# Kernel optimization log

Hardware: AMD Instinct MI355X
Metric: run time of the kernel (lower is better)

## Reference

```python
import jax, jax.numpy as jnp
import numpy as np

BATCH = 16384
IN = 1024
OUT = 1024
SIGMA_MIN = 0.1
SIGMA_MAX = 1.0


def setup_inputs() -> dict:
    key = jax.random.key(0)
    k0, k1, k2, k3 = jax.random.split(key, 4)
    x = jax.random.normal(k0, (BATCH, IN), dtype=jnp.float32)
    # torch init: triu(randn) -> upper-triangular reflector banks
    U = jnp.triu(jax.random.normal(k1, (IN, IN), dtype=jnp.float32))
    V = jnp.triu(jax.random.normal(k2, (OUT, OUT), dtype=jnp.float32))
    p = 0.001 * jax.random.normal(k3, (min(IN, OUT),), dtype=jnp.float32)
    bias = jnp.zeros((OUT,), dtype=jnp.float32)
    return {"x": x, "U": U, "V": V, "p": p, "bias": bias}


def _hprod_step(x, u):
    # u has zeros in its first i entries (triu row i), so the full-vector
    # form equals torch's sliced Hprod on the last k = n - i columns.
    alpha = 2.0 * (x @ u) / jnp.dot(u, u)          # [bs]
    return x - alpha[:, None] * u[None, :], None   # rank-1 update


def reference(x, U, V, p, bias):
    r = (SIGMA_MAX - SIGMA_MIN) / 2.0
    sigma_mean = SIGMA_MIN + r
    # mask enforces torch slice semantics (entries below diag never used)
    Um = U * jnp.triu(jnp.ones_like(U))
    Vm = V * jnp.triu(jnp.ones_like(V))
    # Umultiply: reflectors i = 0 .. n_U-1 in order (sequential recurrence)
    x, _ = jax.lax.scan(_hprod_step, x, Um)
    # Sigma: diagonal scaling (square case IN == OUT)
    sigmas = 2.0 * r * (jax.nn.sigmoid(p) - 0.5) + sigma_mean
    x = x * sigmas[None, :]
    # Vmultiply: reflectors i = n_V-1 .. 0 (reverse order)
    x, _ = jax.lax.scan(_hprod_step, x, Vm[::-1])
    return x + bias
```

## Files before the change

### kernel.cpp

```cpp
#include <hip/hip_runtime.h>
#include <stdint.h>

typedef __attribute__((ext_vector_type(8))) short short8;
typedef __attribute__((ext_vector_type(4))) float f32x4;

#define NN 1024
#define NBATCH 16384
#define ME ((size_t)NN * NN)

__device__ __forceinline__ unsigned short f32_to_bf16_rne(float f) {
  unsigned int u = __float_as_uint(f);
  unsigned int r = (u + 0x7fffu + ((u >> 16) & 1u)) >> 16;
  return (unsigned short)r;
}

__device__ __forceinline__ unsigned int pack2bf(float lo, float hi) {
  return (unsigned int)f32_to_bf16_rne(lo) | ((unsigned int)f32_to_bf16_rne(hi) << 16);
}

__device__ __forceinline__ void split_bf16(float x, unsigned short& h, unsigned short& l) {
  h = f32_to_bf16_rne(x);
  float hf = __uint_as_float((unsigned int)h << 16);
  l = f32_to_bf16_rne(x - hf);
}

__device__ __forceinline__ float allsum64(float x) {
  x += __int_as_float(__builtin_amdgcn_update_dpp(0, __float_as_int(x), 0xB1, 0xF, 0xF, true));
  x += __int_as_float(__builtin_amdgcn_update_dpp(0, __float_as_int(x), 0x4E, 0xF, 0xF, true));
  x += __int_as_float(__builtin_amdgcn_update_dpp(0, __float_as_int(x), 0x141, 0xF, 0xF, true));
  x += __int_as_float(__builtin_amdgcn_update_dpp(0, __float_as_int(x), 0x140, 0xF, 0xF, true));
#if __has_builtin(__builtin_amdgcn_permlane16_swap) && __has_builtin(__builtin_amdgcn_permlane32_swap)
  {
    auto r16 = __builtin_amdgcn_permlane16_swap(__float_as_uint(x), __float_as_uint(x), false, false);
    x = __uint_as_float(r16[0]) + __uint_as_float(r16[1]);
    auto r32 = __builtin_amdgcn_permlane32_swap(__float_as_uint(x), __float_as_uint(x), false, false);
    x = __uint_as_float(r32[0]) + __uint_as_float(r32[1]);
  }
#else
  x += __int_as_float(__builtin_amdgcn_ds_swizzle(__float_as_int(x), 0x401F));
  x += __shfl_xor(x, 32);
#endif
  return x;
}

__global__ __launch_bounds__(256) void prep_kernel(
    const float* __restrict__ U, const float* __restrict__ V,
    const float* __restrict__ p, float* __restrict__ tau_u,
    float* __restrict__ tau_v, float* __restrict__ sigmas) {
  int wave = threadIdx.x >> 6, lane = threadIdx.x & 63;
  int row = blockIdx.x * 4 + wave;
  if (row < 2048) {
    const float* u = (row < NN) ? (U + (size_t)row * NN) : (V + (size_t)(row - NN) * NN);
    float s = 0.f;
#pragma unroll
    for (int t = 0; t < 16; ++t) { float a = u[lane + (t << 6)]; s += a * a; }
    s = allsum64(s);
    if (lane == 0) {
      float tau = 2.0f / s;
      if (row < NN) tau_u[row] = tau;
      else tau_v[row - NN] = tau;
    }
  } else if (row < 2064) {
    int j = ((row - 2048) << 6) + lane;
    float pj = p[j];
    float sg = 1.0f / (1.0f + expf(-pj));
    sigmas[j] = 0.9f * (sg - 0.5f) + 0.55f;
  }
}

__global__ __launch_bounds__(64) void gram_t8_kernel(
    const float* __restrict__ U, const float* __restrict__ V,
    const float* __restrict__ tau_u, const float* __restrict__ tau_v,
    float* __restrict__ T8all) {
  __shared__ float G[64];
  const int blk = blockIdx.x;
  const int lane = threadIdx.x;
  const float* bank;
  int rbase, rsign, st;
  if (blk < 128) { bank = U; rbase = 8 * blk; rsign = 1; st = 8 * blk; }
  else { int s = blk - 128; bank = V; rbase = 1023 - 8 * s; rsign = -1; st = 1016 - 8 * s; }

  if (lane < 28) {
    int j = 1, k = 0, t = lane;
    for (int jj = 1; jj < 8; ++jj) {
      int lo = jj * (jj - 1) / 2, hi = jj * (jj + 1) / 2;
      if (t >= lo && t < hi) { j = jj; k = t - lo; }
    }
    const float* rk = bank + (size_t)(rbase + rsign * k) * NN;
    const float* rj = bank + (size_t)(rbase + rsign * j) * NN;
    float acc = 0.f;
    for (int i = st >> 2; i < 256; ++i) {
      float4 a = *reinterpret_cast<const float4*>(rk + 4 * i);
      float4 b = *reinterpret_cast<const float4*>(rj + 4 * i);
      acc += a.x * b.x + a.y * b.y + a.z * b.z + a.w * b.w;
    }
    G[k * 8 + j] = acc;
  }
  __syncthreads();

  if (lane < 8) {
    float Tr[8];
#pragma unroll
    for (int j = 0; j < 8; ++j) Tr[j] = 0.f;
#pragma unroll
    for (int j = 0; j < 8; ++j) {
      int grow = rbase + rsign * j;
      float tj = (blk < 128) ? tau_u[grow] : tau_v[grow];
      float a = 0.f;
#pragma unroll
      for (int k = 0; k < 8; ++k) {
        if (k < j) a += Tr[k] * G[k * 8 + j];
      }
      Tr[j] = (lane == j) ? tj : (-tj * a);
    }
#pragma unroll
    for (int j = 0; j < 8; ++j) T8all[(size_t)blk * 64 + lane * 8 + j] = Tr[j];
  }
}

__global__ __launch_bounds__(256) void splity_kernel(
    const float* __restrict__ U, const float* __restrict__ V,
    unsigned short* __restrict__ Yhi, unsigned short* __restrict__ Ylo,
    unsigned short* __restrict__ YThi, unsigned short* __restrict__ YTlo) {
  __shared__ float ys[128][129];
  const int tid = threadIdx.x;
  const int c = blockIdx.x >> 3, et = blockIdx.x & 7;
  const int half = tid & 1;
  const int slot = tid >> 1;
  const int e0 = et << 7;
  const int grow = (c < 8) ? ((c << 7) + slot) : (1023 - ((c - 8) << 7) - slot);
  const float* src = ((c < 8) ? U : V) + (size_t)grow * NN + e0 + (half << 6);
#pragma unroll
  for (int i = 0; i < 16; ++i) {
    float4 v4 = *reinterpret_cast<const float4*>(src + (i << 2));
    const int kk = (half << 6) + (i << 2);
    ys[slot][kk + 0] = v4.x; ys[slot][kk + 1] = v4.y;
    ys[slot][kk + 2] = v4.z; ys[slot][kk + 3] = v4.w;
  }
  __syncthreads();
  {
    const size_t rbase = ((size_t)(c * 128 + slot)) * NN + e0 + (half << 6);
#pragma unroll
    for (int i = 0; i < 16; ++i) {
      const int kk = (half << 6) + (i << 2);
      ushort4 h4, l4;
      split_bf16(ys[slot][kk + 0], h4.x, l4.x);
      split_bf16(ys[slot][kk + 1], h4.y, l4.y);
      split_bf16(ys[slot][kk + 2], h4.z, l4.z);
      split_bf16(ys[slot][kk + 3], h4.w, l4.w);
      *reinterpret_cast<ushort4*>(&Yhi[rbase + (i << 2)]) = h4;
      *reinterpret_cast<ushort4*>(&Ylo[rbase + (i << 2)]) = l4;
    }
  }
  {
    const int e = slot;
    const size_t tbase = ((size_t)c * 1024 + e0 + e) * 128 + (half << 6);
#pragma unroll
    for (int i = 0; i < 16; ++i) {
      const int k0 = (half << 6) + (i << 2);
      ushort4 h4, l4;
      split_bf16(ys[k0 + 0][e], h4.x, l4.x);
      split_bf16(ys[k0 + 1][e], h4.y, l4.y);
      split_bf16(ys[k0 + 2][e], h4.z, l4.z);
      split_bf16(ys[k0 + 3][e], h4.w, l4.w);
      *reinterpret_cast<ushort4*>(&YThi[tbase + (i << 2)]) = h4;
      *reinterpret_cast<ushort4*>(&YTlo[tbase + (i << 2)]) = l4;
    }
  }
}

#define LDK 40

__global__ __launch_bounds__(256) void gramt_kernel(
    const unsigned short* __restrict__ Yhi, const unsigned short* __restrict__ Ylo,
    float* __restrict__ G) {
  __shared__ unsigned short Hs[128 * LDK];
  __shared__ unsigned short Ls[128 * LDK];
  const int tid = threadIdx.x;
  const int lane = tid & 63, wave = tid >> 6;
  const int c = blockIdx.x;
  const int wm = wave & 1, wn = wave >> 1;
  const int srow = tid >> 1, scol = (tid & 1) << 4;
  const unsigned short* ph = Yhi + ((size_t)(c * 128 + srow)) * NN + scol;
  const unsigned short* pl = Ylo + ((size_t)(c * 128 + srow)) * NN + scol;

  f32x4 acc[4][4];
#pragma unroll
  for (int a = 0; a < 4; ++a)
#pragma unroll
    for (int b = 0; b < 4; ++b) acc[a][b] = 0.f;

  const int arow0 = wm * 64, brow0 = wn * 64;
  const int fr = lane & 15, kb = (lane >> 4) << 3;

#pragma unroll 1
  for (int kt = 0; kt < 32; ++kt) {
    __syncthreads();
    *reinterpret_cast<uint4*>(&Hs[srow * LDK + scol]) = *reinterpret_cast<const uint4*>(ph + kt * 32);
    *reinterpret_cast<uint4*>(&Hs[srow * LDK + scol + 8]) = *reinterpret_cast<const uint4*>(ph + kt * 32 + 8);
    *reinterpret_cast<uint4*>(&Ls[srow * LDK + scol]) = *reinterpret_cast<const uint4*>(pl + kt * 32);
    *reinterpret_cast<uint4*>(&Ls[srow * LDK + scol + 8]) = *reinterpret_cast<const uint4*>(pl + kt * 32 + 8);
    __syncthreads();
    short8 ah[4], al[4], bh[4], bl[4];
#pragma unroll
    for (int tr = 0; tr < 4; ++tr) {
      ah[tr] = *reinterpret_cast<const short8*>(&Hs[(arow0 + tr * 16 + fr) * LDK + kb]);
      al[tr] = *reinterpret_cast<const short8*>(&Ls[(arow0 + tr * 16 + fr) * LDK + kb]);
    }
#pragma unroll
    for (int tc = 0; tc < 4; ++tc) {
      bh[tc] = *reinterpret_cast<const short8*>(&Hs[(brow0 + tc * 16 + fr) * LDK + kb]);
      bl[tc] = *reinterpret_cast<const short8*>(&Ls[(brow0 + tc * 16 + fr) * LDK + kb]);
    }
#pragma unroll
    for (int tr = 0; tr < 4; ++tr)
#pragma unroll
      for (int tc = 0; tc < 4; ++tc) {
        acc[tr][tc] = __builtin_amdgcn_mfma_f32_16x16x32_bf16(ah[tr], bh[tc], acc[tr][tc], 0, 0, 0);
        acc[tr][tc] = __builtin_amdgcn_mfma_f32_16x16x32_bf16(ah[tr], bl[tc], acc[tr][tc], 0, 0, 0);
        acc[tr][tc] = __builtin_amdgcn_mfma_f32_16x16x32_bf16(al[tr], bh[tc], acc[tr][tc], 0, 0, 0);
      }
  }
  const int rq = (lane >> 4) << 2;
#pragma unroll
  for (int tc = 0; tc < 4; ++tc) {
    const int gc = brow0 + tc * 16 + fr;
#pragma unroll
    for (int tr = 0; tr < 4; ++tr) {
      const int gr = arow0 + tr * 16 + rq;
#pragma unroll
      for (int q = 0; q < 4; ++q)
        G[((size_t)c * 128 + gr + q) * 128 + gc] = acc[tr][tc][q];
    }
  }
}

__global__ __launch_bounds__(256) void ttree_kernel(
    const float* __restrict__ G, const float* __restrict__ T8all,
    unsigned short* __restrict__ Thi, unsigned short* __restrict__ Tlo) {
  __shared__ float Ts[128 * 128];
  __shared__ float Gb[64 * 64];
  __shared__ float Xb[64 * 64];
  const int c = blockIdx.x, tid = threadIdx.x;
  for (int i = tid; i < 128 * 128; i += 256) Ts[i] = 0.f;
  __syncthreads();
  for (int i = tid; i < 1024; i += 256) {
    const int sb = i >> 6, ij = i & 63, r = ij >> 3, col = ij & 7;
    const int t8i = (c < 8) ? (16 * c + sb) : (128 + 16 * (c - 8) + sb);
    Ts[(8 * sb + r) * 128 + 8 * sb + col] = T8all[(size_t)t8i * 64 + ij];
  }
  __syncthreads();
  for (int b = 8; b <= 64; b <<= 1) {
    const int nm = 128 / (2 * b);
    for (int m = 0; m < nm; ++m) {
      const int a0 = 2 * b * m;
      for (int i = tid; i < b * b; i += 256) {
        const int r = i / b, cl = i % b;
        Gb[i] = G[((size_t)c * 128 + a0 + r) * 128 + a0 + b + cl];
      }
      __syncthreads();
      for (int i = tid; i < b * b; i += 256) {
        const int r = i / b, cl = i % b;
        float s = 0.f;
        for (int k = 0; k <= cl; ++k)
          s += Gb[r * b + k] * Ts[(a0 + b + k) * 128 + a0 + b + cl];
        Xb[i] = s;
      }
      __syncthreads();
      for (int i = tid; i < b * b; i += 256) {
        const int r = i / b, cl = i % b;
        float s = 0.f;
        for (int k = r; k < b; ++k)
          s -= Ts[(a0 + r) * 128 + a0 + k] * Xb[k * b + cl];
        Ts[(a0 + r) * 128 + a0 + b + cl] = s;
      }
      __syncthreads();
    }
  }
  for (int i = tid; i < 128 * 128; i += 256) {
    unsigned short h, l;
    split_bf16(Ts[i], h, l);
    Thi[(size_t)c * 128 * 128 + i] = h;
    Tlo[(size_t)c * 128 * 128 + i] = l;
  }
}

__global__ __launch_bounds__(256) void zw_kernel(
    const unsigned short* __restrict__ Thi, const unsigned short* __restrict__ Tlo,
    const unsigned short* __restrict__ YThi, const unsigned short* __restrict__ YTlo,
    unsigned short* __restrict__ WThi, unsigned short* __restrict__ WTlo) {
  __shared__ unsigned short Xh[128 * LDK], Xl[128 * LDK];
  __shared__ unsigned short Wh[128 * LDK], Wl[128 * LDK];
  const int tid = threadIdx.x;
  const int lane = tid & 63, wave = tid >> 6;
  const int c = blockIdx.x >> 3, bn = blockIdx.x & 7;
  const int n0 = bn * 128;
  const int wm = wave & 1, wn = wave >> 1;
  const int srow = tid >> 1, scol = (tid & 1) << 4;
  const unsigned short* pxh = Thi + ((size_t)c * 128 + srow) * 128 + scol;
  const unsigned short* pxl = Tlo + ((size_t)c * 128 + srow) * 128 + scol;
  const unsigned short* pwh = YThi + ((size_t)c * 1024 + n0 + srow) * 128 + scol;
  const unsigned short* pwl = YTlo + ((size_t)c * 1024 + n0 + srow) * 128 + scol;

  f32x4 acc[4][4];
#pragma unroll
  for (int a = 0; a < 4; ++a)
#pragma unroll
    for (int b = 0; b < 4; ++b) acc[a][b] = 0.f;

  const int arow0 = wm * 64, brow0 = wn * 64;
  const int fr = lane & 15, kb = (lane >> 4) << 3;

#pragma unroll 1
  for (int kt = 0; kt < 4; ++kt) {
    __syncthreads();
    *reinterpret_cast<uint4*>(&Xh[srow * LDK + scol]) = *reinterpret_cast<const uint4*>(pxh + kt * 32);
    *reinterpret_cast<uint4*>(&Xh[srow * LDK + scol + 8]) = *reinterpret_cast<const uint4*>(pxh + kt * 32 + 8);
    *reinterpret_cast<uint4*>(&Xl[srow * LDK + scol]) = *reinterpret_cast<const uint4*>(pxl + kt * 32);
    *reinterpret_cast<uint4*>(&Xl[srow * LDK + scol + 8]) = *reinterpret_cast<const uint4*>(pxl + kt * 32 + 8);
    *reinterpret_cast<uint4*>(&Wh[srow * LDK + scol]) = *reinterpret_cast<const uint4*>(pwh + kt * 32);
    *reinterpret_cast<uint4*>(&Wh[srow * LDK + scol + 8]) = *reinterpret_cast<const uint4*>(pwh + kt * 32 + 8);
    *reinterpret_cast<uint4*>(&Wl[srow * LDK + scol]) = *reinterpret_cast<const uint4*>(pwl + kt * 32);
    *reinterpret_cast<uint4*>(&Wl[srow * LDK + scol + 8]) = *reinterpret_cast<const uint4*>(pwl + kt * 32 + 8);
    __syncthreads();
    short8 ah[4], al[4], bh[4], bl[4];
#pragma unroll
    for (int tr = 0; tr < 4; ++tr) {
      ah[tr] = *reinterpret_cast<const short8*>(&Xh[(arow0 + tr * 16 + fr) * LDK + kb]);
      al[tr] = *reinterpret_cast<const short8*>(&Xl[(arow0 + tr * 16 + fr) * LDK + kb]);
    }
#pragma unroll
    for (int tc = 0; tc < 4; ++tc) {
      bh[tc] = *reinterpret_cast<const short8*>(&Wh[(brow0 + tc * 16 + fr) * LDK + kb]);
      bl[tc] = *reinterpret_cast<const short8*>(&Wl[(brow0 + tc * 16 + fr) * LDK + kb]);
    }
#pragma unroll
    for (int tr = 0; tr < 4; ++tr)
#pragma unroll
      for (int tc = 0; tc < 4; ++tc) {
        acc[tr][tc] = __builtin_amdgcn_mfma_f32_16x16x32_bf16(ah[tr], bh[tc], acc[tr][tc], 0, 0, 0);
        acc[tr][tc] = __builtin_amdgcn_mfma_f32_16x16x32_bf16(ah[tr], bl[tc], acc[tr][tc], 0, 0, 0);
        acc[tr][tc] = __builtin_amdgcn_mfma_f32_16x16x32_bf16(al[tr], bh[tc], acc[tr][tc], 0, 0, 0);
      }
  }
  const int rq = (lane >> 4) << 2;
#pragma unroll
  for (int tc = 0; tc < 4; ++tc) {
    const int gc = brow0 + tc * 16 + fr;
#pragma unroll
    for (int tr = 0; tr < 4; ++tr) {
      const int gr = arow0 + tr * 16 + rq;
      ushort4 h4, l4;
      split_bf16(acc[tr][tc][0], h4.x, l4.x);
      split_bf16(acc[tr][tc][1], h4.y, l4.y);
      split_bf16(acc[tr][tc][2], h4.z, l4.z);
      split_bf16(acc[tr][tc][3], h4.w, l4.w);
      const size_t off = ((size_t)c * 1024 + n0 + gc) * 128 + gr;
      *reinterpret_cast<ushort4*>(&WThi[off]) = h4;
      *reinterpret_cast<ushort4*>(&WTlo[off]) = l4;
    }
  }
}

__global__ __launch_bounds__(256) void chainc_kernel(
    const unsigned short* __restrict__ YThi, const unsigned short* __restrict__ YTlo,
    const unsigned short* __restrict__ WThi, const unsigned short* __restrict__ WTlo,
    unsigned short* __restrict__ chains) {
  __shared__ unsigned short Xh[128 * LDK], Xl[128 * LDK];
  __shared__ unsigned short Wh[128 * LDK], Wl[128 * LDK];
  const int tid = threadIdx.x;
  const int lane = tid & 63, wave = tid >> 6;
  const int c = blockIdx.x >> 6, b6 = blockIdx.x & 63;
  const int bm = b6 & 7, bn = b6 >> 3;
  const int m0 = bm * 128, n0 = bn * 128;
  const int wm = wave & 1, wn = wave >> 1;
  const int srow = tid >> 1, scol = (tid & 1) << 4;
  const unsigned short* pxh = YThi + ((size_t)c * 1024 + m0 + srow) * 128 + scol;
  const unsigned short* pxl = YTlo + ((size_t)c * 1024 + m0 + srow) * 128 + scol;
  const unsigned short* pwh = WThi + ((size_t)c * 1024 + n0 + srow) * 128 + scol;
  const unsigned short* pwl = WTlo + ((size_t)c * 1024 + n0 + srow) * 128 + scol;

  f32x4 acc[4][4];
#pragma unroll
  for (int a = 0; a < 4; ++a)
#pragma unroll
    for (int b = 0; b < 4; ++b) acc[a][b] = 0.f;

  const int arow0 = wm * 64, brow0 = wn * 64;
  const int fr = lane & 15, kb = (lane >> 4) << 3;

#pragma unroll 1
  for (int kt = 0; kt < 4; ++kt) {
    __syncthreads();
    *reinterpret_cast<uint4*>(&Xh[srow * LDK + scol]) = *reinterpret_cast<const uint4*>(pxh + kt * 32);
    *reinterpret_cast<uint4*>(&Xh[srow * LDK + scol + 8]) = *reinterpret_cast<const uint4*>(pxh + kt * 32 + 8);
    *reinterpret_cast<uint4*>(&Xl[srow * LDK + scol]) = *reinterpret_cast<const uint4*>(pxl + kt * 32);
    *reinterpret_cast<uint4*>(&Xl[srow * LDK + scol + 8]) = *reinterpret_cast<const uint4*>(pxl + kt * 32 + 8);
    *reinterpret_cast<uint4*>(&Wh[srow * LDK + scol]) = *reinterpret_cast<const uint4*>(pwh + kt * 32);
    *reinterpret_cast<uint4*>(&Wh[srow * LDK + scol + 8]) = *reinterpret_cast<const uint4*>(pwh + kt * 32 + 8);
    *reinterpret_cast<uint4*>(&Wl[srow * LDK + scol]) = *reinterpret_cast<const uint4*>(pwl + kt * 32);
    *reinterpret_cast<uint4*>(&Wl[srow * LDK + scol + 8]) = *reinterpret_cast<const uint4*>(pwl + kt * 32 + 8);
    __syncthreads();
    short8 ah[4], al[4], bh[4], bl[4];
#pragma unroll
    for (int tr = 0; tr < 4; ++tr) {
      ah[tr] = *reinterpret_cast<const short8*>(&Xh[(arow0 + tr * 16 + fr) * LDK + kb]);
      al[tr] = *reinterpret_cast<const short8*>(&Xl[(arow0 + tr * 16 + fr) * LDK + kb]);
    }
#pragma unroll
    for (int tc = 0; tc < 4; ++tc) {
      bh[tc] = *reinterpret_cast<const short8*>(&Wh[(brow0 + tc * 16 + fr) * LDK + kb]);
      bl[tc] = *reinterpret_cast<const short8*>(&Wl[(brow0 + tc * 16 + fr) * LDK + kb]);
    }
#pragma unroll
    for (int tr = 0; tr < 4; ++tr)
#pragma unroll
      for (int tc = 0; tc < 4; ++tc) {
        acc[tr][tc] = __builtin_amdgcn_mfma_f32_16x16x32_bf16(ah[tr], bh[tc], acc[tr][tc], 0, 0, 0);
        acc[tr][tc] = __builtin_amdgcn_mfma_f32_16x16x32_bf16(ah[tr], bl[tc], acc[tr][tc], 0, 0, 0);
        acc[tr][tc] = __builtin_amdgcn_mfma_f32_16x16x32_bf16(al[tr], bh[tc], acc[tr][tc], 0, 0, 0);
      }
  }
  unsigned short* dst = chains + (size_t)c * ME;
  const int rq = (lane >> 4) << 2;
  if ((c & 1) == 0) {
#pragma unroll
    for (int tc = 0; tc < 4; ++tc) {
      const int gcg = n0 + brow0 + tc * 16 + fr;
#pragma unroll
      for (int tr = 0; tr < 4; ++tr) {
        const int grg = m0 + arow0 + tr * 16 + rq;
#pragma unroll
        for (int q = 0; q < 4; ++q) {
          const float val = ((grg + q) == gcg ? 1.0f : 0.0f) - acc[tr][tc][q];
          dst[(size_t)(grg + q) * NN + gcg] = f32_to_bf16_rne(val);
        }
      }
    }
  } else {
#pragma unroll
    for (int tc = 0; tc < 4; ++tc) {
      const int gcg = n0 + brow0 + tc * 16 + fr;
#pragma unroll
      for (int tr = 0; tr < 4; ++tr) {
        const int grg = m0 + arow0 + tr * 16 + rq;
        ushort4 pk;
        pk.x = f32_to_bf16_rne(((grg + 0) == gcg ? 1.0f : 0.0f) - acc[tr][tc][0]);
        pk.y = f32_to_bf16_rne(((grg + 1) == gcg ? 1.0f : 0.0f) - acc[tr][tc][1]);
        pk.z = f32_to_bf16_rne(((grg + 2) == gcg ? 1.0f : 0.0f) - acc[tr][tc][2]);
        pk.w = f32_to_bf16_rne(((grg + 3) == gcg ? 1.0f : 0.0f) - acc[tr][tc][3]);
        *reinterpret_cast<ushort4*>(&dst[(size_t)gcg * NN + grg]) = pk;
      }
    }
  }
}

#define BM 128
#define BN 128
#define BK 32

__device__ __forceinline__ void compose_body(
    const unsigned short* __restrict__ Xb, const unsigned short* __restrict__ Wb,
    unsigned short* __restrict__ Op, const float* __restrict__ sig, int b, bool tstore) {
  __shared__ unsigned short As[BM * LDK];
  __shared__ unsigned short Bs[BN * LDK];
  const int tid = threadIdx.x;
  const int lane = tid & 63, wave = tid >> 6;
  const int bm = b & 7, bn = b >> 3;
  const int m0 = bm * BM, n0 = bn * BN;
  const int wm = wave & 1, wn = wave >> 1;

  const int srow = tid >> 1;
  const int scol = (tid & 1) << 4;
  const unsigned short* aptr = Xb + (size_t)(m0 + srow) * NN + scol;
  const unsigned short* bptr = Wb + (size_t)(n0 + srow) * NN + scol;

  f32x4 acc[4][4];
#pragma unroll
  for (int a = 0; a < 4; ++a)
#pragma unroll
    for (int bb = 0; bb < 4; ++bb) acc[a][bb] = 0.f;

  uint4 ra0 = *reinterpret_cast<const uint4*>(aptr + 0);
  uint4 ra1 = *reinterpret_cast<const uint4*>(aptr + 8);
  uint4 rb0 = *reinterpret_cast<const uint4*>(bptr + 0);
  uint4 rb1 = *reinterpret_cast<const uint4*>(bptr + 8);

  const int arow0 = wm * 64;
  const int brow0 = wn * 64;
  const int fr = lane & 15;
  const int kb = (lane >> 4) << 3;

#pragma unroll 1
  for (int kt = 0; kt < NN / BK; ++kt) {
    __syncthreads();
    *reinterpret_cast<uint4*>(&As[srow * LDK + scol]) = ra0;
    *reinterpret_cast<uint4*>(&As[srow * LDK + scol + 8]) = ra1;
    *reinterpret_cast<uint4*>(&Bs[srow * LDK + scol]) = rb0;
    *reinterpret_cast<uint4*>(&Bs[srow * LDK + scol + 8]) = rb1;
    __syncthreads();
    if (kt + 1 < NN / BK) {
      const unsigned short* ap = aptr + (kt + 1) * BK;
      const unsigned short* bp = bptr + (kt + 1) * BK;
      ra0 = *reinterpret_cast<const uint4*>(ap + 0);
      ra1 = *reinterpret_cast<const uint4*>(ap + 8);
      rb0 = *reinterpret_cast<const uint4*>(bp + 0);
      rb1 = *reinterpret_cast<const uint4*>(bp + 8);
    }
    short8 af[4], bf[4];
#pragma unroll
    for (int tr = 0; tr < 4; ++tr)
      af[tr] = *reinterpret_cast<const short8*>(&As[(arow0 + tr * 16 + fr) * LDK + kb]);
#pragma unroll
    for (int tc = 0; tc < 4; ++tc)
      bf[tc] = *reinterpret_cast<const short8*>(&Bs[(brow0 + tc * 16 + fr) * LDK + kb]);
#pragma unroll
    for (int tr = 0; tr < 4; ++tr)
#pragma unroll
      for (int tc = 0; tc < 4; ++tc)
        acc[tr][tc] = __builtin_amdgcn_mfma_f32_16x16x32_bf16(af[tr], bf[tc], acc[tr][tc], 0, 0, 0);
  }

  const int rq = (lane >> 4) << 2;
  if (!tstore) {
#pragma unroll
    for (int tc = 0; tc < 4; ++tc) {
      const int gc = n0 + brow0 + tc * 16 + fr;
      const float s = sig ? sig[gc] : 1.0f;
#pragma unroll
      for (int tr = 0; tr < 4; ++tr) {
        const int gr = m0 + arow0 + tr * 16 + rq;
#pragma unroll
        for (int q = 0; q < 4; ++q) {
          Op[(size_t)(gr + q) * NN + gc] = f32_to_bf16_rne(acc[tr][tc][q] * s);
        }
      }
    }
  } else {
#pragma unroll
    for (int tc = 0; tc < 4; ++tc) {
      const int gc = n0 + brow0 + tc * 16 + fr;
#pragma unroll
      for (int tr = 0; tr < 4; ++tr) {
        const int gr = m0 + arow0 + tr * 16 + rq;
        ushort4 pk;
        pk.x = f32_to_bf16_rne(acc[tr][tc][0]);
        pk.y = f32_to_bf16_rne(acc[tr][tc][1]);
        pk.z = f32_to_bf16_rne(acc[tr][tc][2]);
        pk.w = f32_to_bf16_rne(acc[tr][tc][3]);
        *reinterpret_cast<ushort4*>(&Op[(size_t)gc * NN + gr]) = pk;
      }
    }
  }
}

__global__ __launch_bounds__(256) void composeL1_kernel(
    const unsigned short* __restrict__ ch, unsigned short* __restrict__ P) {
  const int sub = blockIdx.x >> 6, b = blockIdx.x & 63;
  const int i = sub & 3;
  const unsigned short* x = ch + (size_t)((sub < 4 ? 0 : 8) + 2 * i) * ME;
  compose_body(x, x + ME, P + (size_t)sub * ME, nullptr, b, (i & 1) != 0);
}

__global__ __launch_bounds__(256) void composeL2_kernel(
    const unsigned short* __restrict__ P, unsigned short* __restrict__ Q) {
  const int sub = blockIdx.x >> 6, b = blockIdx.x & 63;
  compose_body(P + (size_t)(2 * sub) * ME, P + (size_t)(2 * sub + 1) * ME,
               Q + (size_t)sub * ME, nullptr, b, (sub & 1) != 0);
}

__global__ __launch_bounds__(256) void composeL3_kernel(
    const unsigned short* __restrict__ Q, const float* __restrict__ sigmas,
    unsigned short* __restrict__ F) {
  const int sub = blockIdx.x >> 6, b = blockIdx.x & 63;
  if (sub == 0) compose_body(Q, Q + ME, F, sigmas, b, false);
  else compose_body(Q + 2 * ME, Q + 3 * ME, F + ME, nullptr, b, true);
}

__global__ __launch_bounds__(256) void composeL4_kernel(
    const unsigned short* __restrict__ F, unsigned short* __restrict__ Mt) {
  compose_body(F + ME, F, Mt, nullptr, blockIdx.x, false);
}

__global__ __launch_bounds__(256) void gemm_kernel(
    const float* __restrict__ X, const unsigned short* __restrict__ Mt,
    const float* __restrict__ bias, float* __restrict__ Out) {
  __shared__ unsigned short As[BM * LDK];
  __shared__ unsigned short Bs[BN * LDK];
  const int tid = threadIdx.x;
  const int lane = tid & 63, wave = tid >> 6;
  const int bm = blockIdx.x & 127;
  const int bn = blockIdx.x >> 7;
  const int m0 = bm * BM, n0 = bn * BN;
  const int wm = wave & 1, wn = wave >> 1;

  const int srow = tid >> 1;
  const int scol = (tid & 1) << 4;
  const float* aptr = X + (size_t)(m0 + srow) * NN + scol;
  const unsigned short* bptr = Mt + (size_t)(n0 + srow) * NN + scol;

  f32x4 acc[4][4];
#pragma unroll
  for (int a = 0; a < 4; ++a)
#pragma unroll
    for (int b = 0; b < 4; ++b) acc[a][b] = 0.f;

  float4 ra0 = *reinterpret_cast<const float4*>(aptr + 0);
  float4 ra1 = *reinterpret_cast<const float4*>(aptr + 4);
  float4 ra2 = *reinterpret_cast<const float4*>(aptr + 8);
  float4 ra3 = *reinterpret_cast<const float4*>(aptr + 12);
  uint4 rb0 = *reinterpret_cast<const uint4*>(bptr + 0);
  uint4 rb1 = *reinterpret_cast<const uint4*>(bptr + 8);

  const int arow0 = wm * 64;
  const int brow0 = wn * 64;
  const int fr = lane & 15;
  const int kb = (lane >> 4) << 3;

#pragma unroll 1
  for (int kt = 0; kt < NN / BK; ++kt) {
    __syncthreads();
    uint4 w0, w1;
    w0.x = pack2bf(ra0.x, ra0.y); w0.y = pack2bf(ra0.z, ra0.w);
    w0.z = pack2bf(ra1.x, ra1.y); w0.w = pack2bf(ra1.z, ra1.w);
    w1.x = pack2bf(ra2.x, ra2.y); w1.y = pack2bf(ra2.z, ra2.w);
    w1.z = pack2bf(ra3.x, ra3.y); w1.w = pack2bf(ra3.z, ra3.w);
    *reinterpret_cast<uint4*>(&As[srow * LDK + scol]) = w0;
    *reinterpret_cast<uint4*>(&As[srow * LDK + scol + 8]) = w1;
    *reinterpret_cast<uint4*>(&Bs[srow * LDK + scol]) = rb0;
    *reinterpret_cast<uint4*>(&Bs[srow * LDK + scol + 8]) = rb1;
    __syncthreads();
    if (kt + 1 < NN / BK) {
      const float* ap = aptr + (kt + 1) * BK;
      const unsigned short* bp = bptr + (kt + 1) * BK;
      ra0 = *reinterpret_cast<const float4*>(ap + 0);
      ra1 = *reinterpret_cast<const float4*>(ap + 4);
      ra2 = *reinterpret_cast<const float4*>(ap + 8);
      ra3 = *reinterpret_cast<const float4*>(ap + 12);
      rb0 = *reinterpret_cast<const uint4*>(bp + 0);
      rb1 = *reinterpret_cast<const uint4*>(bp + 8);
    }
    short8 af[4], bf[4];
#pragma unroll
    for (int tr = 0; tr < 4; ++tr)
      af[tr] = *reinterpret_cast<const short8*>(&As[(arow0 + tr * 16 + fr) * LDK + kb]);
#pragma unroll
    for (int tc = 0; tc < 4; ++tc)
      bf[tc] = *reinterpret_cast<const short8*>(&Bs[(brow0 + tc * 16 + fr) * LDK + kb]);
#pragma unroll
    for (int tr = 0; tr < 4; ++tr)
#pragma unroll
      for (int tc = 0; tc < 4; ++tc)
        acc[tr][tc] = __builtin_amdgcn_mfma_f32_16x16x32_bf16(af[tr], bf[tc], acc[tr][tc], 0, 0, 0);
  }

  const int rq = (lane >> 4) << 2;
#pragma unroll
  for (int tc = 0; tc < 4; ++tc) {
    const int gc = n0 + brow0 + tc * 16 + fr;
    const float bv = bias[gc];
#pragma unroll
    for (int tr = 0; tr < 4; ++tr) {
      const int gr = m0 + arow0 + tr * 16 + rq;
#pragma unroll
      for (int q = 0; q < 4; ++q) {
        Out[(size_t)(gr + q) * NN + gc] = acc[tr][tc][q] + bv;
      }
    }
  }
}

extern "C" void kernel_launch(void* const* d_in, const int* in_sizes, int n_in,
                              void* d_out, int out_size, void* d_ws, size_t ws_size,
                              hipStream_t stream) {
  const float* x = (const float*)d_in[0];
  const float* U = (const float*)d_in[1];
  const float* V = (const float*)d_in[2];
  const float* p = (const float*)d_in[3];
  const float* bias = (const float*)d_in[4];
  float* out = (float*)d_out;

  char* ws = (char*)d_ws;
  float* tau_u = (float*)(ws);
  float* tau_v = (float*)(ws + 4096);
  float* sigmas = (float*)(ws + 8192);
  float* T8all = (float*)(ws + 16384);
  unsigned short* Mt = (unsigned short*)(ws + 81920);

  unsigned short* sc = (unsigned short*)d_out;
  unsigned short* chains = sc;
  unsigned short* P = sc + 16 * ME;
  unsigned short* Q = sc + 24 * ME;
  unsigned short* F = sc + 28 * ME;
  unsigned short* YThi = sc + 16 * ME;
  unsigned short* YTlo = sc + 18 * ME;
  unsigned short* WThi = sc + 20 * ME;
  unsigned short* WTlo = sc + 22 * ME;
  unsigned short* Yhi = sc + 24 * ME;
  unsigned short* Ylo = sc + 26 * ME;
  float* G = (float*)(sc + 28 * ME);
  unsigned short* Thi = sc + 28 * ME + 524288;
  unsigned short* Tlo = Thi + 262144;

  prep_kernel<<<516, 256, 0, stream>>>(U, V, p, tau_u, tau_v, sigmas);
  gram_t8_kernel<<<256, 64, 0, stream>>>(U, V, tau_u, tau_v, T8all);
  splity_kernel<<<128, 256, 0, stream>>>(U, V, Yhi, Ylo, YThi, YTlo);
  gramt_kernel<<<16, 256, 0, stream>>>(Yhi, Ylo, G);
  ttree_kernel<<<16, 256, 0, stream>>>(G, T8all, Thi, Tlo);
  zw_kernel<<<128, 256, 0, stream>>>(Thi, Tlo, YThi, YTlo, WThi, WTlo);
  chainc_kernel<<<1024, 256, 0, stream>>>(YThi, YTlo, WThi, WTlo, chains);
  composeL1_kernel<<<512, 256, 0, stream>>>(chains, P);
  composeL2_kernel<<<256, 256, 0, stream>>>(P, Q);
  composeL3_kernel<<<128, 256, 0, stream>>>(Q, sigmas, F);
  composeL4_kernel<<<64, 256, 0, stream>>>(F, Mt);
  gemm_kernel<<<1024, 256, 0, stream>>>(x, Mt, bias, out);
}
```

Measured before the change: 360.4 us.

## Split-K gram kernel and async double-buffered LDS loads in compose and GEMM

The gram kernel now splits K eight ways across 128 blocks instead of 16, writing partial Gram tiles that ttree sums while loading. The compose and final GEMM kernels replace register-staged LDS copies with direct global-to-LDS loads into double-buffered, XOR-swizzled tiles, dropping one barrier per K step. The GEMM keeps X in fp32 in LDS and converts it to bf16 at fragment-load time. This adds LDS use and conversion work in the inner loop, and it moves Thi into a scratch region that Yhi/Ylo also occupy.

```diff
diff --git a/kernel.cpp b/kernel.cpp
--- a/kernel.cpp
+++ b/kernel.cpp
@@ -170,19 +170,39 @@
 }
 
 #define LDK 40
+#define BM 128
+#define BN 128
+#define BK 32
+
+__device__ __forceinline__ void tile_compute(
+    const unsigned short* __restrict__ As, const unsigned short* __restrict__ Bs,
+    f32x4 acc[4][4], int arow0, int brow0, int fr, int kb) {
+  short8 af[4], bf[4];
+#pragma unroll
+  for (int tr = 0; tr < 4; ++tr)
+    af[tr] = *reinterpret_cast<const short8*>(&As[(arow0 + tr * 16 + fr) * LDK + kb]);
+#pragma unroll
+  for (int tc = 0; tc < 4; ++tc)
+    bf[tc] = *reinterpret_cast<const short8*>(&Bs[(brow0 + tc * 16 + fr) * LDK + kb]);
+#pragma unroll
+  for (int tr = 0; tr < 4; ++tr)
+#pragma unroll
+    for (int tc = 0; tc < 4; ++tc)
+      acc[tr][tc] = __builtin_amdgcn_mfma_f32_16x16x32_bf16(af[tr], bf[tc], acc[tr][tc], 0, 0, 0);
+}
 
 __global__ __launch_bounds__(256) void gramt_kernel(
     const unsigned short* __restrict__ Yhi, const unsigned short* __restrict__ Ylo,
-    float* __restrict__ G) {
+    float* __restrict__ Gp) {
   __shared__ unsigned short Hs[128 * LDK];
   __shared__ unsigned short Ls[128 * LDK];
   const int tid = threadIdx.x;
   const int lane = tid & 63, wave = tid >> 6;
-  const int c = blockIdx.x;
+  const int c = blockIdx.x >> 3, ks = blockIdx.x & 7;
   const int wm = wave & 1, wn = wave >> 1;
   const int srow = tid >> 1, scol = (tid & 1) << 4;
-  const unsigned short* ph = Yhi + ((size_t)(c * 128 + srow)) * NN + scol;
-  const unsigned short* pl = Ylo + ((size_t)(c * 128 + srow)) * NN + scol;
+  const unsigned short* ph = Yhi + ((size_t)(c * 128 + srow)) * NN + ks * 128 + scol;
+  const unsigned short* pl = Ylo + ((size_t)(c * 128 + srow)) * NN + ks * 128 + scol;
 
   f32x4 acc[4][4];
 #pragma unroll
@@ -194,7 +214,7 @@
   const int fr = lane & 15, kb = (lane >> 4) << 3;
 
 #pragma unroll 1
-  for (int kt = 0; kt < 32; ++kt) {
+  for (int kt = 0; kt < 4; ++kt) {
     __syncthreads();
     *reinterpret_cast<uint4*>(&Hs[srow * LDK + scol]) = *reinterpret_cast<const uint4*>(ph + kt * 32);
     *reinterpret_cast<uint4*>(&Hs[srow * LDK + scol + 8]) = *reinterpret_cast<const uint4*>(ph + kt * 32 + 8);
@@ -230,13 +250,13 @@
       const int gr = arow0 + tr * 16 + rq;
 #pragma unroll
       for (int q = 0; q < 4; ++q)
-        G[((size_t)c * 128 + gr + q) * 128 + gc] = acc[tr][tc][q];
+        Gp[(((size_t)c * 8 + ks) * 128 + gr + q) * 128 + gc] = acc[tr][tc][q];
     }
   }
 }
 
 __global__ __launch_bounds__(256) void ttree_kernel(
-    const float* __restrict__ G, const float* __restrict__ T8all,
+    const float* __restrict__ Gp, const float* __restrict__ T8all,
     unsigned short* __restrict__ Thi, unsigned short* __restrict__ Tlo) {
   __shared__ float Ts[128 * 128];
   __shared__ float Gb[64 * 64];
@@ -256,7 +276,11 @@
       const int a0 = 2 * b * m;
       for (int i = tid; i < b * b; i += 256) {
         const int r = i / b, cl = i % b;
-        Gb[i] = G[((size_t)c * 128 + a0 + r) * 128 + a0 + b + cl];
+        float s = 0.f;
+#pragma unroll
+        for (int sl = 0; sl < 8; ++sl)
+          s += Gp[(((size_t)c * 8 + sl) * 128 + a0 + r) * 128 + a0 + b + cl];
+        Gb[i] = s;
       }
       __syncthreads();
       for (int i = tid; i < b * b; i += 256) {
@@ -455,25 +479,56 @@
   }
 }
 
-#define BM 128
-#define BN 128
-#define BK 32
+__device__ __forceinline__ void stage_bf16_tile(
+    const unsigned short* __restrict__ gbase, unsigned short* __restrict__ lds,
+    int tid, int kt) {
+#pragma unroll
+  for (int i = 0; i < 2; ++i) {
+    const int slot = tid + 256 * i;
+    const int row = slot >> 2, s = slot & 3;
+    const int cs = s ^ ((row >> 1) & 3);
+    __builtin_amdgcn_global_load_lds(
+        (const __attribute__((address_space(1))) void*)(gbase + (size_t)row * NN + kt * 32 + cs * 8),
+        (__attribute__((address_space(3))) void*)(lds + row * 32 + s * 8), 16, 0, 0);
+  }
+}
+
+__device__ __forceinline__ void tile_compute32(
+    const unsigned short* __restrict__ As, const unsigned short* __restrict__ Bs,
+    f32x4 acc[4][4], int arow0, int brow0, int fr, int kb) {
+  short8 af[4], bf[4];
+  const int ck = kb >> 3;
+#pragma unroll
+  for (int tr = 0; tr < 4; ++tr) {
+    const int row = arow0 + tr * 16 + fr;
+    const int sl = ck ^ ((row >> 1) & 3);
+    af[tr] = *reinterpret_cast<const short8*>(&As[row * 32 + sl * 8]);
+  }
+#pragma unroll
+  for (int tc = 0; tc < 4; ++tc) {
+    const int row = brow0 + tc * 16 + fr;
+    const int sl = ck ^ ((row >> 1) & 3);
+    bf[tc] = *reinterpret_cast<const short8*>(&Bs[row * 32 + sl * 8]);
+  }
+#pragma unroll
+  for (int tr = 0; tr < 4; ++tr)
+#pragma unroll
+    for (int tc = 0; tc < 4; ++tc)
+      acc[tr][tc] = __builtin_amdgcn_mfma_f32_16x16x32_bf16(af[tr], bf[tc], acc[tr][tc], 0, 0, 0);
+}
 
 __device__ __forceinline__ void compose_body(
     const unsigned short* __restrict__ Xb, const unsigned short* __restrict__ Wb,
     unsigned short* __restrict__ Op, const float* __restrict__ sig, int b, bool tstore) {
-  __shared__ unsigned short As[BM * LDK];
-  __shared__ unsigned short Bs[BN * LDK];
+  __shared__ unsigned short As[2][BM * 32];
+  __shared__ unsigned short Bs[2][BN * 32];
   const int tid = threadIdx.x;
   const int lane = tid & 63, wave = tid >> 6;
   const int bm = b & 7, bn = b >> 3;
   const int m0 = bm * BM, n0 = bn * BN;
   const int wm = wave & 1, wn = wave >> 1;
-
-  const int srow = tid >> 1;
-  const int scol = (tid & 1) << 4;
-  const unsigned short* aptr = Xb + (size_t)(m0 + srow) * NN + scol;
-  const unsigned short* bptr = Wb + (size_t)(n0 + srow) * NN + scol;
+  const int arow0 = wm * 64, brow0 = wn * 64;
+  const int fr = lane & 15, kb = (lane >> 4) << 3;
 
   f32x4 acc[4][4];
 #pragma unroll
@@ -481,44 +536,21 @@
 #pragma unroll
     for (int bb = 0; bb < 4; ++bb) acc[a][bb] = 0.f;
 
-  uint4 ra0 = *reinterpret_cast<const uint4*>(aptr + 0);
-  uint4 ra1 = *reinterpret_cast<const uint4*>(aptr + 8);
-  uint4 rb0 = *reinterpret_cast<const uint4*>(bptr + 0);
-  uint4 rb1 = *reinterpret_cast<const uint4*>(bptr + 8);
-
-  const int arow0 = wm * 64;
-  const int brow0 = wn * 64;
-  const int fr = lane & 15;
-  const int kb = (lane >> 4) << 3;
-
+  const unsigned short* agbase = Xb + (size_t)m0 * NN;
+  const unsigned short* bgbase = Wb + (size_t)n0 * NN;
+
+  stage_bf16_tile(agbase, &As[0][0], tid, 0);
+  stage_bf16_tile(bgbase, &Bs[0][0], tid, 0);
+  int pb = 0;
 #pragma unroll 1
-  for (int kt = 0; kt < NN / BK; ++kt) {
+  for (int kt = 0; kt < 32; ++kt) {
     __syncthreads();
-    *reinterpret_cast<uint4*>(&As[srow * LDK + scol]) = ra0;
-    *reinterpret_cast<uint4*>(&As[srow * LDK + scol + 8]) = ra1;
-    *reinterpret_cast<uint4*>(&Bs[srow * LDK + scol]) = rb0;
-    *reinterpret_cast<uint4*>(&Bs[srow * LDK + scol + 8]) = rb1;
-    __syncthreads();
-    if (kt + 1 < NN / BK) {
-      const unsigned short* ap = aptr + (kt + 1) * BK;
-      const unsigned short* bp = bptr + (kt + 1) * BK;
-      ra0 = *reinterpret_cast<const uint4*>(ap + 0);
-      ra1 = *reinterpret_cast<const uint4*>(ap + 8);
-      rb0 = *reinterpret_cast<const uint4*>(bp + 0);
-      rb1 = *reinterpret_cast<const uint4*>(bp + 8);
-    }
-    short8 af[4], bf[4];
-#pragma unroll
-    for (int tr = 0; tr < 4; ++tr)
-      af[tr] = *reinterpret_cast<const short8*>(&As[(arow0 + tr * 16 + fr) * LDK + kb]);
-#pragma unroll
-    for (int tc = 0; tc < 4; ++tc)
-      bf[tc] = *reinterpret_cast<const short8*>(&Bs[(brow0 + tc * 16 + fr) * LDK + kb]);
-#pragma unroll
-    for (int tr = 0; tr < 4; ++tr)
-#pragma unroll
-      for (int tc = 0; tc < 4; ++tc)
-        acc[tr][tc] = __builtin_amdgcn_mfma_f32_16x16x32_bf16(af[tr], bf[tc], acc[tr][tc], 0, 0, 0);
+    if (kt + 1 < 32) {
+      stage_bf16_tile(agbase, &As[pb ^ 1][0], tid, kt + 1);
+      stage_bf16_tile(bgbase, &Bs[pb ^ 1][0], tid, kt + 1);
+    }
+    tile_compute32(&As[pb][0], &Bs[pb][0], acc, arow0, brow0, fr, kb);
+    pb ^= 1;
   }
 
   const int rq = (lane >> 4) << 2;
@@ -585,19 +617,16 @@
 __global__ __launch_bounds__(256) void gemm_kernel(
     const float* __restrict__ X, const unsigned short* __restrict__ Mt,
     const float* __restrict__ bias, float* __restrict__ Out) {
-  __shared__ unsigned short As[BM * LDK];
-  __shared__ unsigned short Bs[BN * LDK];
+  __shared__ float Af[2][BM * 32];
+  __shared__ unsigned short Bs[2][BN * 32];
   const int tid = threadIdx.x;
   const int lane = tid & 63, wave = tid >> 6;
   const int bm = blockIdx.x & 127;
   const int bn = blockIdx.x >> 7;
   const int m0 = bm * BM, n0 = bn * BN;
   const int wm = wave & 1, wn = wave >> 1;
-
-  const int srow = tid >> 1;
-  const int scol = (tid & 1) << 4;
-  const float* aptr = X + (size_t)(m0 + srow) * NN + scol;
-  const unsigned short* bptr = Mt + (size_t)(n0 + srow) * NN + scol;
+  const int arow0 = wm * 64, brow0 = wn * 64;
+  const int fr = lane & 15, kb = (lane >> 4) << 3;
 
   f32x4 acc[4][4];
 #pragma unroll
@@ -605,54 +634,59 @@
 #pragma unroll
     for (int b = 0; b < 4; ++b) acc[a][b] = 0.f;
 
-  float4 ra0 = *reinterpret_cast<const float4*>(aptr + 0);
-  float4 ra1 = *reinterpret_cast<const float4*>(aptr + 4);
-  float4 ra2 = *reinterpret_cast<const float4*>(aptr + 8);
-  float4 ra3 = *reinterpret_cast<const float4*>(aptr + 12);
-  uint4 rb0 = *reinterpret_cast<const uint4*>(bptr + 0);
-  uint4 rb1 = *reinterpret_cast<const uint4*>(bptr + 8);
-
-  const int arow0 = wm * 64;
-  const int brow0 = wn * 64;
-  const int fr = lane & 15;
-  const int kb = (lane >> 4) << 3;
-
+  const float* agbase = X + (size_t)m0 * NN;
+  const unsigned short* bgbase = Mt + (size_t)n0 * NN;
+
+#define GSTAGE(PB, KT)                                                          \
+  {                                                                             \
+    _Pragma("unroll")                                                           \
+    for (int i = 0; i < 4; ++i) {                                               \
+      const int slot = tid + 256 * i;                                           \
+      const int row = slot >> 3, s = slot & 7;                                  \
+      const int cs = s ^ (row & 7);                                             \
+      __builtin_amdgcn_global_load_lds(                                         \
+          (const __attribute__((address_space(1))) void*)(agbase + (size_t)row * NN + (KT) * 32 + cs * 4), \
+          (__attribute__((address_space(3))) void*)(&Af[PB][row * 32 + s * 4]), 16, 0, 0); \
+    }                                                                           \
+    stage_bf16_tile(bgbase, &Bs[PB][0], tid, KT);                               \
+  }
+
+  GSTAGE(0, 0)
+  int pb = 0;
 #pragma unroll 1
-  for (int kt = 0; kt < NN / BK; ++kt) {
+  for (int kt = 0; kt < 32; ++kt) {
     __syncthreads();
-    uint4 w0, w1;
-    w0.x = pack2bf(ra0.x, ra0.y); w0.y = pack2bf(ra0.z, ra0.w);
-    w0.z = pack2bf(ra1.x, ra1.y); w0.w = pack2bf(ra1.z, ra1.w);
-    w1.x = pack2bf(ra2.x, ra2.y); w1.y = pack2bf(ra2.z, ra2.w);
-    w1.z = pack2bf(ra3.x, ra3.y); w1.w = pack2bf(ra3.z, ra3.w);
-    *reinterpret_cast<uint4*>(&As[srow * LDK + scol]) = w0;
-    *reinterpret_cast<uint4*>(&As[srow * LDK + scol + 8]) = w1;
-    *reinterpret_cast<uint4*>(&Bs[srow * LDK + scol]) = rb0;
-    *reinterpret_cast<uint4*>(&Bs[srow * LDK + scol + 8]) = rb1;
-    __syncthreads();
-    if (kt + 1 < NN / BK) {
-      const float* ap = aptr + (kt + 1) * BK;
-      const unsigned short* bp = bptr + (kt + 1) * BK;
-      ra0 = *reinterpret_cast<const float4*>(ap + 0);
-      ra1 = *reinterpret_cast<const float4*>(ap + 4);
-      ra2 = *reinterpret_cast<const float4*>(ap + 8);
-      ra3 = *reinterpret_cast<const float4*>(ap + 12);
-      rb0 = *reinterpret_cast<const uint4*>(bp + 0);
-      rb1 = *reinterpret_cast<const uint4*>(bp + 8);
-    }
-    short8 af[4], bf[4];
-#pragma unroll
-    for (int tr = 0; tr < 4; ++tr)
-      af[tr] = *reinterpret_cast<const short8*>(&As[(arow0 + tr * 16 + fr) * LDK + kb]);
-#pragma unroll
-    for (int tc = 0; tc < 4; ++tc)
-      bf[tc] = *reinterpret_cast<const short8*>(&Bs[(brow0 + tc * 16 + fr) * LDK + kb]);
-#pragma unroll
-    for (int tr = 0; tr < 4; ++tr)
-#pragma unroll
-      for (int tc = 0; tc < 4; ++tc)
-        acc[tr][tc] = __builtin_amdgcn_mfma_f32_16x16x32_bf16(af[tr], bf[tc], acc[tr][tc], 0, 0, 0);
-  }
+    if (kt + 1 < 32) GSTAGE(pb ^ 1, kt + 1)
+    {
+      short8 af[4], bf[4];
+      const int c0 = kb >> 2;
+      const int ckb = kb >> 3;
+#pragma unroll
+      for (int tr = 0; tr < 4; ++tr) {
+        const int row = arow0 + tr * 16 + fr;
+        const int s0 = c0 ^ (row & 7), s1 = (c0 + 1) ^ (row & 7);
+        const f32x4 a0 = *reinterpret_cast<const f32x4*>(&Af[pb][row * 32 + s0 * 4]);
+        const f32x4 a1 = *reinterpret_cast<const f32x4*>(&Af[pb][row * 32 + s1 * 4]);
+        uint4 w;
+        w.x = pack2bf(a0[0], a0[1]); w.y = pack2bf(a0[2], a0[3]);
+        w.z = pack2bf(a1[0], a1[1]); w.w = pack2bf(a1[2], a1[3]);
+        af[tr] = *reinterpret_cast<const short8*>(&w);
+      }
+#pragma unroll
+      for (int tc = 0; tc < 4; ++tc) {
+        const int row = brow0 + tc * 16 + fr;
+        const int sl = ckb ^ ((row >> 1) & 3);
+        bf[tc] = *reinterpret_cast<const short8*>(&Bs[pb][row * 32 + sl * 8]);
+      }
+#pragma unroll
+      for (int tr = 0; tr < 4; ++tr)
+#pragma unroll
+        for (int tc = 0; tc < 4; ++tc)
+          acc[tr][tc] = __builtin_amdgcn_mfma_f32_16x16x32_bf16(af[tr], bf[tc], acc[tr][tc], 0, 0, 0);
+    }
+    pb ^= 1;
+  }
+#undef GSTAGE
 
   const int rq = (lane >> 4) << 2;
 #pragma unroll
@@ -698,15 +732,15 @@
   unsigned short* WTlo = sc + 22 * ME;
   unsigned short* Yhi = sc + 24 * ME;
   unsigned short* Ylo = sc + 26 * ME;
-  float* G = (float*)(sc + 28 * ME);
-  unsigned short* Thi = sc + 28 * ME + 524288;
+  float* Gp = (float*)(sc + 28 * ME);
+  unsigned short* Thi = sc + 24 * ME;
   unsigned short* Tlo = Thi + 262144;
 
   prep_kernel<<<516, 256, 0, stream>>>(U, V, p, tau_u, tau_v, sigmas);
   gram_t8_kernel<<<256, 64, 0, stream>>>(U, V, tau_u, tau_v, T8all);
   splity_kernel<<<128, 256, 0, stream>>>(U, V, Yhi, Ylo, YThi, YTlo);
-  gramt_kernel<<<16, 256, 0, stream>>>(Yhi, Ylo, G);
-  ttree_kernel<<<16, 256, 0, stream>>>(G, T8all, Thi, Tlo);
+  gramt_kernel<<<128, 256, 0, stream>>>(Yhi, Ylo, Gp);
+  ttree_kernel<<<16, 256, 0, stream>>>(Gp, T8all, Thi, Tlo);
   zw_kernel<<<128, 256, 0, stream>>>(Thi, Tlo, YThi, YTlo, WThi, WTlo);
   chainc_kernel<<<1024, 256, 0, stream>>>(YThi, YTlo, WThi, WTlo, chains);
   composeL1_kernel<<<512, 256, 0, stream>>>(chains, P);
```

After: 347.1 us. -3.7%, faster.
